# Kernel tuning notes

Hardware: AMD Instinct MI355X
Metric: run time of the kernel (lower is better)

Reference implementation:

```python
import jax, jax.numpy as jnp
import numpy as np

EMBED = 1024
HEADS = 16
HEAD_DIM = EMBED // HEADS
RANK = 8
ALPHA = 16
SCALE_LORA = ALPHA / RANK  # 2.0


def _lora_linear(x, W, b, A, B):
    # F.linear(x, W, b) + scale * F.linear(F.linear(x, A), B)
    return x @ W.T + b + SCALE_LORA * ((x @ A.T) @ B.T)


def setup_inputs() -> dict:
    key = jax.random.key(0)
    ks = jax.random.split(key, 17)
    d = {"x": jax.random.normal(ks[0], (2, 2048, EMBED), dtype=jnp.float32)}
    names = ["q", "k", "v", "o"]
    i = 1
    for n in names:
        d[f"W{n}"] = jax.random.normal(ks[i], (EMBED, EMBED), dtype=jnp.float32) * 0.02; i += 1
        d[f"b{n}"] = jnp.zeros((EMBED,), dtype=jnp.float32)
        d[f"A{n}"] = jax.random.normal(ks[i], (RANK, EMBED), dtype=jnp.float32) * 0.02; i += 1
        d[f"B{n}"] = jax.random.normal(ks[i], (EMBED, RANK), dtype=jnp.float32) * 0.02; i += 1
    return d


def reference(x, Wq, bq, Aq, Bq, Wk, bk, Ak, Bk, Wv, bv, Av, Bv, Wo, bo, Ao, Bo):
    N, S, _ = x.shape
    Q = _lora_linear(x, Wq, bq, Aq, Bq).reshape(N, S, HEADS, HEAD_DIM)
    K = _lora_linear(x, Wk, bk, Ak, Bk).reshape(N, S, HEADS, HEAD_DIM)
    V = _lora_linear(x, Wv, bv, Av, Bv).reshape(N, S, HEADS, HEAD_DIM)
    # energy: [N, H, Sq, Sk]
    energy = jnp.einsum("nqhd,nkhd->nhqk", Q, K) / jnp.sqrt(jnp.float32(HEAD_DIM))
    attn = jax.nn.softmax(energy, axis=-1)
    out = jnp.einsum("nhqk,nkhd->nqhd", attn, V).reshape(N, S, EMBED)
    return _lora_linear(out, Wo, bo, Ao, Bo)
```

## Files before the change

kernel.cpp:

```cpp
#include <hip/hip_runtime.h>
#include <stdint.h>

typedef uint16_t u16;
typedef short s16x8 __attribute__((ext_vector_type(8)));
typedef float f32x4 __attribute__((ext_vector_type(4)));
typedef unsigned short u16x4 __attribute__((ext_vector_type(4)));
typedef uint32_t u32;
typedef u32 u32x2 __attribute__((ext_vector_type(2)));
typedef u32 u32x4 __attribute__((ext_vector_type(4)));

#define MFMA16(a,b,c) __builtin_amdgcn_mfma_f32_16x16x32_bf16((a),(b),(c),0,0,0)
#define QSCALE 0.18033688011112042f

__device__ __forceinline__ float b2f(u16 b){
  union { u32 u; float f; } v; v.u = ((u32)b)<<16; return v.f;
}
__device__ __forceinline__ u16 f2b(float f){
  union { float f; u32 u; } v; v.f = f;
  return (u16)((v.u + 0x7fffu + ((v.u>>16)&1u))>>16);
}
__device__ __forceinline__ u32 fbits(float f){
  union { float f; u32 u; } v; v.f = f; return v.u;
}
__device__ __forceinline__ void load_lds_16B(const void* g, void* l){
  __builtin_amdgcn_global_load_lds((const __attribute__((address_space(1))) void*)g,
                                   (__attribute__((address_space(3))) void*)l, 16, 0, 0);
}

template<bool XF32, int NMAT>
__global__ __launch_bounds__(256) void lora_conv_kernel(
    const void* __restrict__ Xv,
    const float* __restrict__ A0, const float* __restrict__ A1, const float* __restrict__ A2,
    float* __restrict__ T0, float* __restrict__ T1, float* __restrict__ T2,
    u16* __restrict__ xb,
    const float* __restrict__ W0, const float* __restrict__ W1,
    const float* __restrict__ W2, const float* __restrict__ W3,
    u16* __restrict__ Wb)
{
  if (XF32 && blockIdx.x >= 1024){
    const int cv = blockIdx.x - 1024;
    const int y = cv>>8;
    const float* src = (y==0)?W0:(y==1)?W1:(y==2)?W2:W3;
    u16* dst = Wb + (size_t)y*1048576;
    const int g = (cv&255)*256 + threadIdx.x;
#pragma unroll
    for (int t=0;t<4;t++){
      const int i4 = g + t*65536;
      const f32x4 v = *(const f32x4*)(src + (size_t)i4*4);
      u16x4 o;
#pragma unroll
      for (int j=0;j<4;j++) o[j] = f2b(v[j]);
      *(u16x4*)(dst + (size_t)i4*4) = o;
    }
    return;
  }

  const int wid = threadIdx.x>>6, lane = threadIdx.x&63;
  const int m = blockIdx.x*4 + wid;

  float xf[16];
  if (XF32){
    const float* xp = (const float*)Xv + (size_t)m*1024 + lane*16;
#pragma unroll
    for (int q=0;q<4;q++){
      const f32x4 v = *(const f32x4*)(xp + q*4);
#pragma unroll
      for (int j=0;j<4;j++) xf[q*4+j] = v[j];
    }
    u16* xbp = xb + (size_t)m*1024 + lane*16;
#pragma unroll
    for (int q=0;q<4;q++){
      u16x4 o;
#pragma unroll
      for (int j=0;j<4;j++) o[j] = f2b(xf[q*4+j]);
      *(u16x4*)(xbp + q*4) = o;
    }
  } else {
    const u16* xp = (const u16*)Xv + (size_t)m*1024 + lane*16;
#pragma unroll
    for (int j=0;j<16;j++) xf[j] = b2f(xp[j]);
  }

#pragma unroll
  for (int mat=0; mat<NMAT; mat++){
    const float* A = (mat==0)?A0:(mat==1)?A1:A2;
    float* T = (mat==0)?T0:(mat==1)?T1:T2;
    float accv[8];
#pragma unroll
    for (int r=0;r<8;r++){
      const float* ap = A + r*1024 + lane*16;
      float s = 0.f;
#pragma unroll
      for (int q=0;q<4;q++){
        const f32x4 av = *(const f32x4*)(ap + q*4);
#pragma unroll
        for (int j=0;j<4;j++) s += xf[q*4+j]*av[j];
      }
      accv[r] = s;
    }
#pragma unroll
    for (int r=0;r<8;r++){
      float s = accv[r];
      s += __shfl_xor(s,1);  s += __shfl_xor(s,2);  s += __shfl_xor(s,4);
      s += __shfl_xor(s,8);  s += __shfl_xor(s,16); s += __shfl_xor(s,32);
      accv[r] = s;
    }
    if (lane==0){
#pragma unroll
      for (int r=0;r<8;r++) T[(size_t)m*8 + r] = accv[r];
    }
  }
}

__global__ __launch_bounds__(256,2) void gemm_qkv_kernel(
    const u16* __restrict__ Xb, const u16* __restrict__ Wb,
    const float* __restrict__ bq, const float* __restrict__ bk, const float* __restrict__ bv,
    const float* __restrict__ tq, const float* __restrict__ tk, const float* __restrict__ tv,
    const float* __restrict__ Blq, const float* __restrict__ Blk, const float* __restrict__ Blv,
    u16* __restrict__ Qb, u16* __restrict__ Kb, u16* __restrict__ Vtb)
{
  __shared__ u16 At[128*32];
  __shared__ u16 Bt[128*32];
  const int tid = threadIdx.x;
  const int wid = tid>>6, lane = tid&63;
  const int quad = lane>>4, l16 = lane&15;
  const int wm = wid>>1, wn = wid&1;
  const int proj = blockIdx.x>>3;
  const int n0 = (blockIdx.x&7)<<7, m0 = blockIdx.y<<7;
  const u16* W = Wb + (size_t)proj*1048576;
  const float* bias = (proj==0)?bq:(proj==1)?bk:bv;
  const float* T    = (proj==0)?tq:(proj==1)?tk:tv;
  const float* Bl   = (proj==0)?Blq:(proj==1)?Blk:Blv;
  const float scale = (proj==0)?QSCALE:1.0f;

  f32x4 acc[4][4];
#pragma unroll
  for (int i=0;i<4;i++)
#pragma unroll
    for (int j=0;j<4;j++) acc[i][j] = f32x4{0.f,0.f,0.f,0.f};

  for (int k0=0;k0<1024;k0+=32){
#pragma unroll
    for (int p=0;p<2;p++){
      const int s = wid*128 + p*64 + lane;
      const int row = s>>2, c = s&3;
      load_lds_16B(Xb + (size_t)(m0+row)*1024 + k0 + c*8, At + (wid*128+p*64)*8);
      load_lds_16B(W  + (size_t)(n0+row)*1024 + k0 + c*8, Bt + (wid*128+p*64)*8);
    }
    __syncthreads();
    s16x8 af[4], bfr[4];
#pragma unroll
    for (int t=0;t<4;t++){
      const int r = wm*64 + t*16 + l16;
      af[t]  = *(const s16x8*)(At + r*32 + quad*8);
      const int c = wn*64 + t*16 + l16;
      bfr[t] = *(const s16x8*)(Bt + c*32 + quad*8);
    }
#pragma unroll
    for (int tm=0;tm<4;tm++)
#pragma unroll
      for (int tn=0;tn<4;tn++)
        acc[tm][tn] = MFMA16(af[tm], bfr[tn], acc[tm][tn]);
    __syncthreads();
  }

  s16x8 tf[4], bfl[4];
#pragma unroll
  for (int t=0;t<4;t++){ tf[t] = s16x8{0,0,0,0,0,0,0,0}; bfl[t] = s16x8{0,0,0,0,0,0,0,0}; }
  if (quad==0){
#pragma unroll
    for (int tm=0;tm<4;tm++){
      const float* tp = T + (size_t)(m0 + wm*64 + tm*16 + l16)*8;
      const f32x4 a0 = *(const f32x4*)(tp);
      const f32x4 a1 = *(const f32x4*)(tp+4);
#pragma unroll
      for (int j=0;j<4;j++){ tf[tm][j] = (short)f2b(2.0f*a0[j]); tf[tm][4+j] = (short)f2b(2.0f*a1[j]); }
    }
#pragma unroll
    for (int tn=0;tn<4;tn++){
      const float* bp = Bl + (size_t)(n0 + wn*64 + tn*16 + l16)*8;
      const f32x4 b0 = *(const f32x4*)(bp);
      const f32x4 b1 = *(const f32x4*)(bp+4);
#pragma unroll
      for (int j=0;j<4;j++){ bfl[tn][j] = (short)f2b(b0[j]); bfl[tn][4+j] = (short)f2b(b1[j]); }
    }
  }
#pragma unroll
  for (int tm=0;tm<4;tm++)
#pragma unroll
    for (int tn=0;tn<4;tn++)
      acc[tm][tn] = MFMA16(tf[tm], bfl[tn], acc[tm][tn]);

#pragma unroll
  for (int tn=0;tn<4;tn++){
    const int n = n0 + wn*64 + tn*16 + l16;
    const float bn = bias[n];
#pragma unroll
    for (int tm=0;tm<4;tm++){
      const int mb = m0 + wm*64 + tm*16 + quad*4;
      if (proj==0){
#pragma unroll
        for (int rg=0;rg<4;rg++) Qb[(size_t)(mb+rg)*1024 + n] = f2b((acc[tm][tn][rg]+bn)*scale);
      } else if (proj==1){
#pragma unroll
        for (int rg=0;rg<4;rg++) Kb[(size_t)(mb+rg)*1024 + n] = f2b(acc[tm][tn][rg]+bn);
      } else {
        const int batch = mb>>11, sI = mb&2047;
        const int hh = n>>6, dd = n&63;
        u16x4 pk;
#pragma unroll
        for (int rg=0;rg<4;rg++) pk[rg] = f2b(acc[tm][tn][rg]+bn);
        *(u16x4*)(Vtb + (size_t)((batch*16+hh)*64+dd)*2048 + sI) = pk;
      }
    }
  }
}

__global__ __launch_bounds__(256,2) void gemm_o_kernel(
    const u16* __restrict__ Xb, const u16* __restrict__ W,
    const float* __restrict__ bias, const float* __restrict__ T,
    const float* __restrict__ Bl, float* __restrict__ Out)
{
  __shared__ u16 At[128*32];
  __shared__ u16 Bt[64*32];
  const int tid = threadIdx.x;
  const int wid = tid>>6, lane = tid&63;
  const int quad = lane>>4, l16 = lane&15;
  const int wm = wid>>1, wn = wid&1;
  const int m0 = blockIdx.y<<7, n0 = blockIdx.x<<6;

  f32x4 acc[4][2];
#pragma unroll
  for (int i=0;i<4;i++)
#pragma unroll
    for (int j=0;j<2;j++) acc[i][j] = f32x4{0.f,0.f,0.f,0.f};

  for (int k0=0;k0<1024;k0+=32){
#pragma unroll
    for (int p=0;p<2;p++){
      const int s = wid*128 + p*64 + lane;
      const int row = s>>2, c = s&3;
      load_lds_16B(Xb + (size_t)(m0+row)*1024 + k0 + c*8, At + (wid*128+p*64)*8);
    }
    { const int s = wid*64 + lane;
      const int row = s>>2, c = s&3;
      load_lds_16B(W + (size_t)(n0+row)*1024 + k0 + c*8, Bt + (wid*64)*8); }
    __syncthreads();
    s16x8 af[4], bfr[2];
#pragma unroll
    for (int t=0;t<4;t++){
      const int r = wm*64 + t*16 + l16;
      af[t] = *(const s16x8*)(At + r*32 + quad*8);
    }
#pragma unroll
    for (int t=0;t<2;t++){
      const int c = wn*32 + t*16 + l16;
      bfr[t] = *(const s16x8*)(Bt + c*32 + quad*8);
    }
#pragma unroll
    for (int tm=0;tm<4;tm++)
#pragma unroll
      for (int tn=0;tn<2;tn++)
        acc[tm][tn] = MFMA16(af[tm], bfr[tn], acc[tm][tn]);
    __syncthreads();
  }

  s16x8 tf[4], bfl[2];
#pragma unroll
  for (int t=0;t<4;t++) tf[t] = s16x8{0,0,0,0,0,0,0,0};
#pragma unroll
  for (int t=0;t<2;t++) bfl[t] = s16x8{0,0,0,0,0,0,0,0};
  if (quad==0){
#pragma unroll
    for (int tm=0;tm<4;tm++){
      const float* tp = T + (size_t)(m0 + wm*64 + tm*16 + l16)*8;
      const f32x4 a0 = *(const f32x4*)(tp);
      const f32x4 a1 = *(const f32x4*)(tp+4);
#pragma unroll
      for (int j=0;j<4;j++){ tf[tm][j] = (short)f2b(2.0f*a0[j]); tf[tm][4+j] = (short)f2b(2.0f*a1[j]); }
    }
#pragma unroll
    for (int tn=0;tn<2;tn++){
      const float* bp = Bl + (size_t)(n0 + wn*32 + tn*16 + l16)*8;
      const f32x4 b0 = *(const f32x4*)(bp);
      const f32x4 b1 = *(const f32x4*)(bp+4);
#pragma unroll
      for (int j=0;j<4;j++){ bfl[tn][j] = (short)f2b(b0[j]); bfl[tn][4+j] = (short)f2b(b1[j]); }
    }
  }
#pragma unroll
  for (int tm=0;tm<4;tm++)
#pragma unroll
    for (int tn=0;tn<2;tn++)
      acc[tm][tn] = MFMA16(tf[tm], bfl[tn], acc[tm][tn]);

#pragma unroll
  for (int tn=0;tn<2;tn++){
    const int n = n0 + wn*32 + tn*16 + l16;
    const float bn = bias[n];
#pragma unroll
    for (int tm=0;tm<4;tm++){
      const int mb = m0 + wm*64 + tm*16 + quad*4;
#pragma unroll
      for (int rg=0;rg<4;rg++)
        Out[(size_t)(mb+rg)*1024 + n] = acc[tm][tn][rg] + bn;
    }
  }
}

__global__ __launch_bounds__(512,4) void attn_kernel(
    const u16* __restrict__ Q, const u16* __restrict__ K,
    const u16* __restrict__ Vt, u16* __restrict__ Out)
{
  __shared__ u16 KtB[2][128*72];
  __shared__ u16 VtB[2][64*136];
  const int tid = threadIdx.x;
  const int wid = tid>>6, lane = tid&63;
  const int quad = lane>>4, l16 = lane&15;
  const int q0 = blockIdx.x<<7;
  const int h = blockIdx.y, nb = blockIdx.z;
  const int qg = wid>>1;
  const int kh = wid&1;
  const int qw = qg*32;

  s16x8 qf[2][2];
#pragma unroll
  for (int g=0;g<2;g++){
    const int row = q0 + qw + g*16 + l16;
#pragma unroll
    for (int dh=0;dh<2;dh++)
      qf[g][dh] = *(const s16x8*)(Q + (size_t)(nb*2048+row)*1024 + h*64 + dh*32 + quad*8);
  }
  f32x4 OT[2][4];
  f32x4 Lacc[2];
#pragma unroll
  for (int g=0;g<2;g++){
#pragma unroll
    for (int td=0;td<4;td++) OT[g][td] = f32x4{0.f,0.f,0.f,0.f};
    Lacc[g] = f32x4{0.f,0.f,0.f,0.f};
  }
  s16x8 ones;
#pragma unroll
  for (int j=0;j<8;j++) ones[j] = (short)0x3F80;

  s16x8 kreg[2], vreg[2];
  auto LOADT = [&](int kn){
#pragma unroll
    for (int p=0;p<2;p++){
      const int s = p*512 + tid;
      kreg[p] = *(const s16x8*)(K + (size_t)(nb*2048+kn+(s>>3))*1024 + h*64 + (s&7)*8);
      vreg[p] = *(const s16x8*)(Vt + (size_t)((nb*16+h)*64+(s>>4))*2048 + kn + (s&15)*8);
    }
  };
  auto WRITET = [&](int b){
    u16* Ktb = KtB[b]; u16* Vtb = VtB[b];
#pragma unroll
    for (int p=0;p<2;p++){
      const int s = p*512 + tid;
      *(s16x8*)(Ktb + (s>>3)*72 + (s&7)*8) = kreg[p];
      *(s16x8*)(Vtb + (s>>4)*136 + (s&15)*8) = vreg[p];
    }
  };

  LOADT(0);
  WRITET(0);
  LOADT(128);
  __syncthreads();

  for (int t=0;t<16;t++){
    const int cur = t&1;
    if (t < 15) WRITET(cur^1);
    if (t < 14) LOADT((t+2)*128);
    const u16* KtC = KtB[cur];
    const u16* VtC = VtB[cur];

#pragma unroll
    for (int kb=0;kb<2;kb++){
      u32 ew[2][2], ow[2][2];
#pragma unroll
      for (int sel=0;sel<2;sel++){
        const int key = kh*64 + kb*32 + sel*16 + l16;
        const s16x8 kf0 = *(const s16x8*)(KtC + key*72 + quad*8);
        const s16x8 kf1 = *(const s16x8*)(KtC + key*72 + 32 + quad*8);
#pragma unroll
        for (int g=0;g<2;g++){
          f32x4 z = f32x4{0.f,0.f,0.f,0.f};
          z = MFMA16(kf0, qf[g][0], z);
          z = MFMA16(kf1, qf[g][1], z);
          const float p0 = __builtin_amdgcn_exp2f(z[0]);
          const float p1 = __builtin_amdgcn_exp2f(z[1]);
          const float p2 = __builtin_amdgcn_exp2f(z[2]);
          const float p3 = __builtin_amdgcn_exp2f(z[3]);
          const u32 w0 = __builtin_amdgcn_perm(fbits(p1), fbits(p0), 0x07060302u);
          const u32 w1 = __builtin_amdgcn_perm(fbits(p3), fbits(p2), 0x07060302u);
          if (sel==0){ ew[g][0]=w0; ew[g][1]=w1; } else { ow[g][0]=w0; ow[g][1]=w1; }
        }
      }
      s16x8 pf[2];
#pragma unroll
      for (int g=0;g<2;g++){
        const u32x2 r32 = __builtin_amdgcn_permlane32_swap(ew[g][0], ow[g][0], false, false);
        const u32x2 r16 = __builtin_amdgcn_permlane16_swap(r32[0], r32[1], false, false);
        const u32x2 s32 = __builtin_amdgcn_permlane32_swap(ew[g][1], ow[g][1], false, false);
        const u32x2 s16v = __builtin_amdgcn_permlane16_swap(s32[0], s32[1], false, false);
        u32x4 pw; pw[0]=r16[0]; pw[1]=s16v[0]; pw[2]=r16[1]; pw[3]=s16v[1];
        pf[g] = __builtin_bit_cast(s16x8, pw);
      }
      __builtin_amdgcn_s_setprio(1);
#pragma unroll
      for (int td=0;td<4;td++){
        const s16x8 vf = *(const s16x8*)(VtC + (td*16+l16)*136 + kh*64 + kb*32 + quad*8);
#pragma unroll
        for (int g=0;g<2;g++)
          OT[g][td] = MFMA16(vf, pf[g], OT[g][td]);
      }
#pragma unroll
      for (int g=0;g<2;g++)
        Lacc[g] = MFMA16(ones, pf[g], Lacc[g]);
      __builtin_amdgcn_s_setprio(0);
    }
    __syncthreads();
  }

  float* ep = (float*)KtB;
  float* lw = (float*)VtB;
  if (kh==1){
#pragma unroll
    for (int g=0;g<2;g++){
      const int q = qw + g*16 + l16;
#pragma unroll
      for (int td=0;td<4;td++)
        *(f32x4*)(ep + q*68 + td*16 + quad*4) = OT[g][td];
      if (quad==0) lw[q] = Lacc[g][0];
    }
  }
  __syncthreads();
  if (kh==0){
#pragma unroll
    for (int g=0;g<2;g++){
      const int q = qw + g*16 + l16;
      const float linv = 1.0f / (Lacc[g][0] + lw[q]);
      const int qout = q0 + q;
#pragma unroll
      for (int td=0;td<4;td++){
        const f32x4 o2 = *(const f32x4*)(ep + q*68 + td*16 + quad*4);
        u16x4 pk;
#pragma unroll
        for (int rg=0;rg<4;rg++) pk[rg] = f2b((OT[g][td][rg]+o2[rg])*linv);
        *(u16x4*)(Out + (size_t)(nb*2048+qout)*1024 + h*64 + td*16 + quad*4) = pk;
      }
    }
  }
}

extern "C" void kernel_launch(void* const* d_in, const int* in_sizes, int n_in,
                              void* d_out, int out_size, void* d_ws, size_t ws_size,
                              hipStream_t stream)
{
  const float* x  = (const float*)d_in[0];
  const float* Wq = (const float*)d_in[1];  const float* bq = (const float*)d_in[2];
  const float* Aq = (const float*)d_in[3];  const float* Bq = (const float*)d_in[4];
  const float* Wk = (const float*)d_in[5];  const float* bk = (const float*)d_in[6];
  const float* Ak = (const float*)d_in[7];  const float* Bk = (const float*)d_in[8];
  const float* Wv = (const float*)d_in[9];  const float* bv = (const float*)d_in[10];
  const float* Av = (const float*)d_in[11]; const float* Bv = (const float*)d_in[12];
  const float* Wo = (const float*)d_in[13]; const float* bo = (const float*)d_in[14];
  const float* Ao = (const float*)d_in[15]; const float* Bo = (const float*)d_in[16];

  char* ws = (char*)d_ws;
  float* tq = (float*)(ws + 0);
  float* tk = (float*)(ws + 131072);
  float* tv = (float*)(ws + 262144);
  float* to = (float*)(ws + 393216);
  u16* xb  = (u16*)(ws + 524288);
  u16* Ab  = xb;
  u16* Wb  = (u16*)(ws + 524288 + 8388608);
  u16* Qb  = (u16*)(ws + 524288 + 2*8388608);
  u16* Kb  = (u16*)(ws + 524288 + 3*8388608);
  u16* Vtb = (u16*)(ws + 524288 + 4*8388608);

  lora_conv_kernel<true,3><<<dim3(2048),256,0,stream>>>(
      x, Aq, Ak, Av, tq, tk, tv, xb, Wq, Wk, Wv, Wo, Wb);
  gemm_qkv_kernel<<<dim3(24,32),256,0,stream>>>(xb, Wb, bq, bk, bv, tq, tk, tv,
                                                Bq, Bk, Bv, Qb, Kb, Vtb);
  attn_kernel<<<dim3(16,16,2),512,0,stream>>>(Qb, Kb, Vtb, Ab);
  lora_conv_kernel<false,1><<<dim3(1024),256,0,stream>>>(
      Ab, Ao, Ao, Ao, to, to, to, nullptr,
      nullptr, nullptr, nullptr, nullptr, nullptr);
  gemm_o_kernel<<<dim3(16,32),256,0,stream>>>(Ab, Wb + (size_t)3*1048576, bo, to, Bo,
                                              (float*)d_out);
}
```

Measured before the change: 238.6 us.

## Fuse output LoRA-A projection into attention epilogue and deepen GEMM K-steps

The separate lora_conv pass over the attention output is removed. The attention kernel's epilogue now computes the rank-8 projection of each head slice and accumulates it into the output T buffer with atomicAdd. That buffer is zeroed in the first conversion kernel. Both GEMM kernels also load two 32-wide K slices per barrier pair (K step 64 with doubled LDS), which halves the number of syncs. The trade-off is extra LDS, lower occupancy headroom, and float atomics across 16 heads, which make the result nondeterministic.

```diff
diff --git a/kernel.cpp b/kernel.cpp
--- a/kernel.cpp
+++ b/kernel.cpp
@@ -27,18 +27,18 @@
                                    (__attribute__((address_space(3))) void*)l, 16, 0, 0);
 }
 
-template<bool XF32, int NMAT>
 __global__ __launch_bounds__(256) void lora_conv_kernel(
-    const void* __restrict__ Xv,
+    const float* __restrict__ x,
     const float* __restrict__ A0, const float* __restrict__ A1, const float* __restrict__ A2,
     float* __restrict__ T0, float* __restrict__ T1, float* __restrict__ T2,
     u16* __restrict__ xb,
     const float* __restrict__ W0, const float* __restrict__ W1,
     const float* __restrict__ W2, const float* __restrict__ W3,
-    u16* __restrict__ Wb)
+    u16* __restrict__ Wb, float* __restrict__ toz)
 {
-  if (XF32 && blockIdx.x >= 1024){
+  if (blockIdx.x >= 1024){
     const int cv = blockIdx.x - 1024;
+    if (threadIdx.x < 32) toz[cv*32 + threadIdx.x] = 0.f;
     const int y = cv>>8;
     const float* src = (y==0)?W0:(y==1)?W1:(y==2)?W2:W3;
     u16* dst = Wb + (size_t)y*1048576;
@@ -59,8 +59,8 @@
   const int m = blockIdx.x*4 + wid;
 
   float xf[16];
-  if (XF32){
-    const float* xp = (const float*)Xv + (size_t)m*1024 + lane*16;
+  {
+    const float* xp = x + (size_t)m*1024 + lane*16;
 #pragma unroll
     for (int q=0;q<4;q++){
       const f32x4 v = *(const f32x4*)(xp + q*4);
@@ -75,14 +75,10 @@
       for (int j=0;j<4;j++) o[j] = f2b(xf[q*4+j]);
       *(u16x4*)(xbp + q*4) = o;
     }
-  } else {
-    const u16* xp = (const u16*)Xv + (size_t)m*1024 + lane*16;
-#pragma unroll
-    for (int j=0;j<16;j++) xf[j] = b2f(xp[j]);
-  }
-
-#pragma unroll
-  for (int mat=0; mat<NMAT; mat++){
+  }
+
+#pragma unroll
+  for (int mat=0; mat<3; mat++){
     const float* A = (mat==0)?A0:(mat==1)?A1:A2;
     float* T = (mat==0)?T0:(mat==1)?T1:T2;
     float accv[8];
@@ -119,8 +115,8 @@
     const float* __restrict__ Blq, const float* __restrict__ Blk, const float* __restrict__ Blv,
     u16* __restrict__ Qb, u16* __restrict__ Kb, u16* __restrict__ Vtb)
 {
-  __shared__ u16 At[128*32];
-  __shared__ u16 Bt[128*32];
+  __shared__ u16 At[2][128*32];
+  __shared__ u16 Bt[2][128*32];
   const int tid = threadIdx.x;
   const int wid = tid>>6, lane = tid&63;
   const int quad = lane>>4, l16 = lane&15;
@@ -139,28 +135,34 @@
 #pragma unroll
     for (int j=0;j<4;j++) acc[i][j] = f32x4{0.f,0.f,0.f,0.f};
 
-  for (int k0=0;k0<1024;k0+=32){
-#pragma unroll
-    for (int p=0;p<2;p++){
-      const int s = wid*128 + p*64 + lane;
-      const int row = s>>2, c = s&3;
-      load_lds_16B(Xb + (size_t)(m0+row)*1024 + k0 + c*8, At + (wid*128+p*64)*8);
-      load_lds_16B(W  + (size_t)(n0+row)*1024 + k0 + c*8, Bt + (wid*128+p*64)*8);
+  for (int k0=0;k0<1024;k0+=64){
+#pragma unroll
+    for (int half=0; half<2; half++){
+#pragma unroll
+      for (int p=0;p<2;p++){
+        const int s = wid*128 + p*64 + lane;
+        const int row = s>>2, c = s&3;
+        load_lds_16B(Xb + (size_t)(m0+row)*1024 + k0 + half*32 + c*8, At[half] + (wid*128+p*64)*8);
+        load_lds_16B(W  + (size_t)(n0+row)*1024 + k0 + half*32 + c*8, Bt[half] + (wid*128+p*64)*8);
+      }
     }
     __syncthreads();
-    s16x8 af[4], bfr[4];
-#pragma unroll
-    for (int t=0;t<4;t++){
-      const int r = wm*64 + t*16 + l16;
-      af[t]  = *(const s16x8*)(At + r*32 + quad*8);
-      const int c = wn*64 + t*16 + l16;
-      bfr[t] = *(const s16x8*)(Bt + c*32 + quad*8);
-    }
-#pragma unroll
-    for (int tm=0;tm<4;tm++)
-#pragma unroll
-      for (int tn=0;tn<4;tn++)
-        acc[tm][tn] = MFMA16(af[tm], bfr[tn], acc[tm][tn]);
+#pragma unroll
+    for (int half=0; half<2; half++){
+      s16x8 af[4], bfr[4];
+#pragma unroll
+      for (int t=0;t<4;t++){
+        const int r = wm*64 + t*16 + l16;
+        af[t]  = *(const s16x8*)(At[half] + r*32 + quad*8);
+        const int c = wn*64 + t*16 + l16;
+        bfr[t] = *(const s16x8*)(Bt[half] + c*32 + quad*8);
+      }
+#pragma unroll
+      for (int tm=0;tm<4;tm++)
+#pragma unroll
+        for (int tn=0;tn<4;tn++)
+          acc[tm][tn] = MFMA16(af[tm], bfr[tn], acc[tm][tn]);
+    }
     __syncthreads();
   }
 
@@ -221,8 +223,8 @@
     const float* __restrict__ bias, const float* __restrict__ T,
     const float* __restrict__ Bl, float* __restrict__ Out)
 {
-  __shared__ u16 At[128*32];
-  __shared__ u16 Bt[64*32];
+  __shared__ u16 At[2][128*32];
+  __shared__ u16 Bt[2][64*32];
   const int tid = threadIdx.x;
   const int wid = tid>>6, lane = tid&63;
   const int quad = lane>>4, l16 = lane&15;
@@ -235,33 +237,39 @@
 #pragma unroll
     for (int j=0;j<2;j++) acc[i][j] = f32x4{0.f,0.f,0.f,0.f};
 
-  for (int k0=0;k0<1024;k0+=32){
-#pragma unroll
-    for (int p=0;p<2;p++){
-      const int s = wid*128 + p*64 + lane;
-      const int row = s>>2, c = s&3;
-      load_lds_16B(Xb + (size_t)(m0+row)*1024 + k0 + c*8, At + (wid*128+p*64)*8);
-    }
-    { const int s = wid*64 + lane;
-      const int row = s>>2, c = s&3;
-      load_lds_16B(W + (size_t)(n0+row)*1024 + k0 + c*8, Bt + (wid*64)*8); }
+  for (int k0=0;k0<1024;k0+=64){
+#pragma unroll
+    for (int half=0; half<2; half++){
+#pragma unroll
+      for (int p=0;p<2;p++){
+        const int s = wid*128 + p*64 + lane;
+        const int row = s>>2, c = s&3;
+        load_lds_16B(Xb + (size_t)(m0+row)*1024 + k0 + half*32 + c*8, At[half] + (wid*128+p*64)*8);
+      }
+      { const int s = wid*64 + lane;
+        const int row = s>>2, c = s&3;
+        load_lds_16B(W + (size_t)(n0+row)*1024 + k0 + half*32 + c*8, Bt[half] + (wid*64)*8); }
+    }
     __syncthreads();
-    s16x8 af[4], bfr[2];
-#pragma unroll
-    for (int t=0;t<4;t++){
-      const int r = wm*64 + t*16 + l16;
-      af[t] = *(const s16x8*)(At + r*32 + quad*8);
-    }
-#pragma unroll
-    for (int t=0;t<2;t++){
-      const int c = wn*32 + t*16 + l16;
-      bfr[t] = *(const s16x8*)(Bt + c*32 + quad*8);
-    }
-#pragma unroll
-    for (int tm=0;tm<4;tm++)
-#pragma unroll
-      for (int tn=0;tn<2;tn++)
-        acc[tm][tn] = MFMA16(af[tm], bfr[tn], acc[tm][tn]);
+#pragma unroll
+    for (int half=0; half<2; half++){
+      s16x8 af[4], bfr[2];
+#pragma unroll
+      for (int t=0;t<4;t++){
+        const int r = wm*64 + t*16 + l16;
+        af[t] = *(const s16x8*)(At[half] + r*32 + quad*8);
+      }
+#pragma unroll
+      for (int t=0;t<2;t++){
+        const int c = wn*32 + t*16 + l16;
+        bfr[t] = *(const s16x8*)(Bt[half] + c*32 + quad*8);
+      }
+#pragma unroll
+      for (int tm=0;tm<4;tm++)
+#pragma unroll
+        for (int tn=0;tn<2;tn++)
+          acc[tm][tn] = MFMA16(af[tm], bfr[tn], acc[tm][tn]);
+    }
     __syncthreads();
   }
 
@@ -310,7 +318,8 @@
 
 __global__ __launch_bounds__(512,4) void attn_kernel(
     const u16* __restrict__ Q, const u16* __restrict__ K,
-    const u16* __restrict__ Vt, u16* __restrict__ Out)
+    const u16* __restrict__ Vt, u16* __restrict__ Out,
+    const float* __restrict__ Ao, float* __restrict__ to)
 {
   __shared__ u16 KtB[2][128*72];
   __shared__ u16 VtB[2][64*136];
@@ -441,13 +450,30 @@
       const int q = qw + g*16 + l16;
       const float linv = 1.0f / (Lacc[g][0] + lw[q]);
       const int qout = q0 + q;
+      float obf[4][4];
 #pragma unroll
       for (int td=0;td<4;td++){
         const f32x4 o2 = *(const f32x4*)(ep + q*68 + td*16 + quad*4);
         u16x4 pk;
 #pragma unroll
-        for (int rg=0;rg<4;rg++) pk[rg] = f2b((OT[g][td][rg]+o2[rg])*linv);
+        for (int rg=0;rg<4;rg++){
+          pk[rg] = f2b((OT[g][td][rg]+o2[rg])*linv);
+          obf[td][rg] = b2f(pk[rg]);
+        }
         *(u16x4*)(Out + (size_t)(nb*2048+qout)*1024 + h*64 + td*16 + quad*4) = pk;
+      }
+#pragma unroll
+      for (int r=0;r<8;r++){
+        float s = 0.f;
+#pragma unroll
+        for (int td=0;td<4;td++){
+          const f32x4 av = *(const f32x4*)(Ao + r*1024 + h*64 + td*16 + quad*4);
+#pragma unroll
+          for (int rg=0;rg<4;rg++) s += obf[td][rg]*av[rg];
+        }
+        s += __shfl_xor(s,16);
+        s += __shfl_xor(s,32);
+        if (quad==0) atomicAdd(to + (size_t)(nb*2048+qout)*8 + r, s);
       }
     }
   }
@@ -479,14 +505,11 @@
   u16* Kb  = (u16*)(ws + 524288 + 3*8388608);
   u16* Vtb = (u16*)(ws + 524288 + 4*8388608);
 
-  lora_conv_kernel<true,3><<<dim3(2048),256,0,stream>>>(
-      x, Aq, Ak, Av, tq, tk, tv, xb, Wq, Wk, Wv, Wo, Wb);
+  lora_conv_kernel<<<dim3(2048),256,0,stream>>>(
+      x, Aq, Ak, Av, tq, tk, tv, xb, Wq, Wk, Wv, Wo, Wb, to);
   gemm_qkv_kernel<<<dim3(24,32),256,0,stream>>>(xb, Wb, bq, bk, bv, tq, tk, tv,
                                                 Bq, Bk, Bv, Qb, Kb, Vtb);
-  attn_kernel<<<dim3(16,16,2),512,0,stream>>>(Qb, Kb, Vtb, Ab);
-  lora_conv_kernel<false,1><<<dim3(1024),256,0,stream>>>(
-      Ab, Ao, Ao, Ao, to, to, to, nullptr,
-      nullptr, nullptr, nullptr, nullptr, nullptr);
+  attn_kernel<<<dim3(16,16,2),512,0,stream>>>(Qb, Kb, Vtb, Ab, Ao, to);
   gemm_o_kernel<<<dim3(16,32),256,0,stream>>>(Ab, Wb + (size_t)3*1048576, bo, to, Bo,
                                               (float*)d_out);
 }
```

New measurement: 232.2 us. -2.7%, faster.
